# Performance work log

Hardware: AMD Instinct MI355X
Metric: run time of the kernel (lower is better)

## Reference

```python
import jax, jax.numpy as jnp
import numpy as np
from jax import lax

B, L, G, D = 32, 1024, 3, 384
H = D // 4  # hidden of attention MLPs
EPS = 1e-5


def _ln(x, g, b):
    m = x.mean(-1, keepdims=True)
    v = ((x - m) ** 2).mean(-1, keepdims=True)
    return (x - m) / jnp.sqrt(v + EPS) * g + b


def _mlp(x, W1, b1, g, beta, W2, b2):
    h = jax.nn.relu(_ln(x @ W1 + b1, g, beta))
    return h @ W2 + b2


def _forward(x, mg_W1, mg_b1, mg_g, mg_beta, mg_W2, mg_b2,
             ph_W1, ph_b1, ph_g, ph_beta, ph_W2, ph_b2,
             bd_W1, bd_b1, bd_g, bd_beta, bd_W2, bd_b2,
             cg_W1, cg_b1, cg_g, cg_beta, cg_W2, cg_b2,
             conv_W, conv_b):
    cls_tok, seq = x[:, :1, :], x[:, 1:, :]
    b = seq.shape[0]
    xg = seq.reshape(b, G, L, D)
    glob = xg.mean(axis=1, keepdims=True)                       # [b,1,L,D]
    gate_in = jnp.concatenate([xg, jnp.broadcast_to(glob, xg.shape)], axis=-1)
    gate = jax.nn.sigmoid(_mlp(gate_in, cg_W1, cg_b1, cg_g, cg_beta, cg_W2, cg_b2))  # [b,G,L,1]
    xg = xg * gate + glob * (1.0 - gate)
    # Conv2d(dim, dim, (3,1), padding=(1,0)) on [b, D, G, L]
    xc = jnp.transpose(xg, (0, 3, 1, 2))
    xc = lax.conv_general_dilated(xc, conv_W, (1, 1), ((1, 1), (0, 0)),
                                  dimension_numbers=('NCHW', 'OIHW', 'NCHW'))
    xc = xc + conv_b[None, :, None, None]
    xg = jnp.transpose(xc, (0, 2, 3, 1))                        # [b,G,L,D]
    # FFT over patch dim (vectorized over groups instead of Python loop)
    fft = jnp.fft.fft(xg, axis=2)
    mag = jnp.abs(fft)
    phase = jnp.angle(fft)
    freq = jnp.abs(jnp.fft.fftfreq(L) * L)
    r1, r2 = L // 8, L // 4
    masks = jnp.stack([(freq <= r1), (freq > r1) & (freq <= r2), (freq > r2)]).astype(mag.dtype)  # [3,L]
    bw = jax.nn.softmax(_mlp(xg.mean(axis=2), bd_W1, bd_b1, bd_g, bd_beta, bd_W2, bd_b2), axis=-1)  # [b,G,3]
    wm = jnp.einsum('bgi,il->bgl', bw, masks)[..., None]        # sum_i mask_i*band_weight_i
    mag_att = jax.nn.sigmoid(_mlp(mag, mg_W1, mg_b1, mg_g, mg_beta, mg_W2, mg_b2))
    ph_att = jnp.tanh(_mlp(phase, ph_W1, ph_b1, ph_g, ph_beta, ph_W2, ph_b2))
    mag_out = mag * wm * mag_att
    ph_out = phase * wm + ph_att
    comp = lax.complex(mag_out * jnp.cos(ph_out), mag_out * jnp.sin(ph_out))
    out = jnp.fft.ifft(comp, axis=2).real.astype(x.dtype)       # [b,G,L,D]
    out = out.reshape(b, G * L, D)
    return jnp.concatenate([cls_tok, out], axis=1)


def setup_inputs() -> dict:
    key = jax.random.key(0)
    ks = jax.random.split(key, 16)
    s = 0.02
    d = {
        'x': jax.random.normal(ks[0], (B, 1 + G * L, D), jnp.float32),
        'mg_W1': jax.random.normal(ks[1], (D, H)) * s, 'mg_b1': jnp.zeros((H,)),
        'mg_g': jnp.ones((H,)), 'mg_beta': jnp.zeros((H,)),
        'mg_W2': jax.random.normal(ks[2], (H, D)) * s, 'mg_b2': jnp.zeros((D,)),
        'ph_W1': jax.random.normal(ks[3], (D, H)) * s, 'ph_b1': jnp.zeros((H,)),
        'ph_g': jnp.ones((H,)), 'ph_beta': jnp.zeros((H,)),
        'ph_W2': jax.random.normal(ks[4], (H, D)) * s, 'ph_b2': jnp.zeros((D,)),
        'bd_W1': jax.random.normal(ks[5], (D, H)) * s, 'bd_b1': jnp.zeros((H,)),
        'bd_g': jnp.ones((H,)), 'bd_beta': jnp.zeros((H,)),
        'bd_W2': jax.random.normal(ks[6], (H, 3)) * s, 'bd_b2': jnp.zeros((3,)),
        'cg_W1': jax.random.normal(ks[7], (2 * D, D // 2)) * s, 'cg_b1': jnp.zeros((D // 2,)),
        'cg_g': jnp.ones((D // 2,)), 'cg_beta': jnp.zeros((D // 2,)),
        'cg_W2': jax.random.normal(ks[8], (D // 2, 1)) * s, 'cg_b2': jnp.zeros((1,)),
        'conv_W': jax.random.normal(ks[9], (D, D, 3, 1)) * s, 'conv_b': jnp.zeros((D,)),
    }
    return d


def reference(x, mg_W1, mg_b1, mg_g, mg_beta, mg_W2, mg_b2,
              ph_W1, ph_b1, ph_g, ph_beta, ph_W2, ph_b2,
              bd_W1, bd_b1, bd_g, bd_beta, bd_W2, bd_b2,
              cg_W1, cg_b1, cg_g, cg_beta, cg_W2, cg_b2,
              conv_W, conv_b):
    return _forward(x, mg_W1, mg_b1, mg_g, mg_beta, mg_W2, mg_b2,
                    ph_W1, ph_b1, ph_g, ph_beta, ph_W2, ph_b2,
                    bd_W1, bd_b1, bd_g, bd_beta, bd_W2, bd_b2,
                    cg_W1, cg_b1, cg_g, cg_beta, cg_W2, cg_b2,
                    conv_W, conv_b)
```

## Files before the change

### kernel.cpp

```cpp
#include <hip/hip_runtime.h>
#include <hip/hip_bf16.h>
#include <hip/hip_fp16.h>
#include <math.h>

#define NB 32
#define NL 1024
#define NG 3
#define ND 384
#define NH 96
#define NDG 192
#define SEQR 3073

typedef __attribute__((ext_vector_type(8))) short short8n;
typedef __attribute__((ext_vector_type(4))) short short4n;
typedef __attribute__((ext_vector_type(8))) _Float16 half8n;
typedef __attribute__((ext_vector_type(4))) float f32x4;
typedef __attribute__((ext_vector_type(4))) unsigned int uint4n;

__device__ __forceinline__ short bfx(float f) {
  __hip_bfloat16 h = __float2bfloat16(f);
  return *reinterpret_cast<short*>(&h);
}
__device__ __forceinline__ float xbf(short s) {
  __hip_bfloat16 h = *reinterpret_cast<__hip_bfloat16*>(&s);
  return __bfloat162float(h);
}
__device__ __forceinline__ short hfx(float f) {
  __half h = __float2half(f);
  return *reinterpret_cast<short*>(&h);
}
__device__ __forceinline__ float xhf(short s) {
  __half h = *reinterpret_cast<__half*>(&s);
  return __half2float(h);
}

__device__ __forceinline__ float fast_atan2f(float y, float x) {
  float ax = fabsf(x), ay = fabsf(y);
  float mx = fmaxf(ax, ay), mn = fminf(ax, ay);
  float r = (mx == 0.0f) ? 0.0f : __fdividef(mn, mx);
  float s = r * r;
  float p = fmaf(s, 0.0208351f, -0.0851330f);
  p = fmaf(s, p, 0.1801410f);
  p = fmaf(s, p, -0.3302995f);
  p = fmaf(s, p, 0.9998660f);
  p = r * p;
  float a = (ay > ax) ? (1.5707963267948966f - p) : p;
  a = (x < 0.0f) ? (3.14159265358979323846f - a) : a;
  return (y < 0.0f) ? -a : a;
}

__device__ __forceinline__ float fast_sigmoid(float x) {
  return __fdividef(1.0f, 1.0f + __expf(-x));
}
__device__ __forceinline__ float fast_tanh(float x) {
  return 1.0f - __fdividef(2.0f, 1.0f + __expf(2.0f * x));
}

__device__ __forceinline__ int swzd(int p) { return p + (p >> 5); }
__device__ __forceinline__ int swzt(int t) { return t + (t >> 4); }

__device__ __forceinline__ int rev4_10(int p) {
  unsigned q = (unsigned)p, r = 0;
#pragma unroll
  for (int i = 0; i < 5; i++) { r = (r << 2) | (q & 3); q >>= 2; }
  return (int)r;
}

__global__ __launch_bounds__(256) void k_prep(const float* __restrict__ convW,
                                              const float* __restrict__ x,
                                              const float* __restrict__ mgW1s,
                                              const float* __restrict__ phW1s,
                                              const float* __restrict__ mgW2s,
                                              const float* __restrict__ phW2s,
                                              const float* __restrict__ cgW1s,
                                              __hip_bfloat16* __restrict__ Wt2,
                                              float* __restrict__ twid,
                                              __half* __restrict__ W1Ao,
                                              __half* __restrict__ W2Ao,
                                              __hip_bfloat16* __restrict__ W1Go,
                                              float* __restrict__ outp) {
  int id = blockIdx.x * 256 + threadIdx.x;
  if (id < 384 * 384 * 3) {
    int i = id % 384; int rest = id / 384; int o = rest % 384; int kh = rest / 384;
    Wt2[id] = __float2bfloat16(convW[(o * 384 + i) * 3 + kh]);
    return;
  }
  int id2 = id - 384 * 384 * 3;
  if (id2 < 1024) {
    float ang = -6.283185307179586f * (float)id2 / 1024.0f;
    float s, c; sincosf(ang, &s, &c);
    twid[2 * id2] = c; twid[2 * id2 + 1] = s;
    return;
  }
  int id3 = id2 - 1024;
  if (id3 < NB * ND) {
    int b = id3 / ND, d = id3 % ND;
    outp[(size_t)b * SEQR * ND + d] = x[(size_t)b * SEQR * ND + d];
    return;
  }
  int id4 = id3 - NB * ND;
  if (id4 < 2 * 36864) {
    int br = id4 / 36864, idx = id4 % 36864;
    int j = idx & 7, ln = (idx >> 3) & 63, rest = idx >> 9;
    int f = rest % 6, kk = rest / 6;
    int m = f * 16 + (ln & 15), k = kk * 32 + (ln >> 4) * 8 + j;
    const float* W = br ? phW1s : mgW1s;
    W1Ao[id4] = __float2half(W[k * NH + m]);
    return;
  }
  int id5 = id4 - 2 * 36864;
  if (id5 < 2 * 36864) {
    int br = id5 / 36864, idx = id5 % 36864;
    int j = idx & 7, ln = (idx >> 3) & 63, rest = idx >> 9;
    int f = rest % 24, kk = rest / 24;
    int d = f * 16 + (ln & 15), k = kk * 32 + (ln >> 4) * 8 + j;
    const float* W = br ? phW2s : mgW2s;
    W2Ao[id5] = __float2half(W[k * ND + d]);
    return;
  }
  int id6 = id5 - 2 * 36864;
  if (id6 < 147456) {
    int j = id6 & 7, ln = (id6 >> 3) & 63, rest = id6 >> 9;
    int f = rest % 12, rest2 = rest / 12;
    int kk = rest2 % 12, part = rest2 / 12;
    int m = f * 16 + (ln & 15), k = part * 384 + kk * 32 + (ln >> 4) * 8 + j;
    W1Go[id6] = __float2bfloat16(cgW1s[k * NDG + m]);
  }
}

__global__ __launch_bounds__(256) void k_gate2(const float* __restrict__ x,
    const __hip_bfloat16* __restrict__ W1G,
    const float* __restrict__ b1, const float* __restrict__ gam,
    const float* __restrict__ bet, const float* __restrict__ W2,
    const float* __restrict__ b2p,
    __hip_bfloat16* __restrict__ gatedA) {
  int bid = blockIdx.x;
  int b = bid >> 6; int l0 = (bid & 63) * 16;
  int tid = threadIdx.x;
  int lane = tid & 63, wid = tid >> 6;
  int r15 = lane & 15, kc = lane >> 4;

  __shared__ short xs[3][16][392];
  __shared__ short gs[16][392];
  __shared__ float hG[16][196];
  __shared__ float s_b1[NDG], s_g[NDG], s_be[NDG], s_w2[NDG];
  __shared__ float sgate[3][16];

  if (tid < NDG) {
    s_b1[tid] = b1[tid]; s_g[tid] = gam[tid];
    s_be[tid] = bet[tid]; s_w2[tid] = W2[tid];
  }
  for (int c = tid; c < 16 * 96; c += 256) {
    int l = c / 96, d4 = (c % 96) * 4;
    size_t base = ((size_t)b * SEQR + 1 + l0 + l) * ND + d4;
    float4 v0 = *reinterpret_cast<const float4*>(&x[base]);
    float4 v1 = *reinterpret_cast<const float4*>(&x[base + (size_t)NL * ND]);
    float4 v2 = *reinterpret_cast<const float4*>(&x[base + (size_t)2 * NL * ND]);
    short4n q0, q1, q2, qg;
    q0.x = bfx(v0.x); q0.y = bfx(v0.y); q0.z = bfx(v0.z); q0.w = bfx(v0.w);
    q1.x = bfx(v1.x); q1.y = bfx(v1.y); q1.z = bfx(v1.z); q1.w = bfx(v1.w);
    q2.x = bfx(v2.x); q2.y = bfx(v2.y); q2.z = bfx(v2.z); q2.w = bfx(v2.w);
    qg.x = bfx((v0.x + v1.x + v2.x) * (1.0f / 3.0f));
    qg.y = bfx((v0.y + v1.y + v2.y) * (1.0f / 3.0f));
    qg.z = bfx((v0.z + v1.z + v2.z) * (1.0f / 3.0f));
    qg.w = bfx((v0.w + v1.w + v2.w) * (1.0f / 3.0f));
    *reinterpret_cast<short4n*>(&xs[0][l][d4]) = q0;
    *reinterpret_cast<short4n*>(&xs[1][l][d4]) = q1;
    *reinterpret_cast<short4n*>(&xs[2][l][d4]) = q2;
    *reinterpret_cast<short4n*>(&gs[l][d4]) = qg;
  }
  __syncthreads();

  const short* bsrc = (wid == 3) ? &gs[0][0] : &xs[wid][0][0];
  const __hip_bfloat16* W1b = W1G + (size_t)(wid == 3 ? 1 : 0) * 73728;
  f32x4 hacc[12];
#pragma unroll
  for (int f = 0; f < 12; f++)
#pragma unroll
    for (int j = 0; j < 4; j++)
      hacc[f][j] = (wid == 3) ? 0.0f : s_b1[f * 16 + kc * 4 + j];
  for (int kk = 0; kk < 12; kk++) {
    short8n bx = *reinterpret_cast<const short8n*>(&bsrc[r15 * 392 + kk * 32 + kc * 8]);
#pragma unroll
    for (int f = 0; f < 12; f++) {
      short8n aw = *reinterpret_cast<const short8n*>(
          (const void*)(W1b + (((size_t)kk * 12 + f) * 64 + lane) * 8));
      hacc[f] = __builtin_amdgcn_mfma_f32_16x16x32_bf16(aw, bx, hacc[f], 0, 0, 0);
    }
  }
  if (wid == 3) {
#pragma unroll
    for (int f = 0; f < 12; f++)
#pragma unroll
      for (int j = 0; j < 4; j++)
        hG[r15][f * 16 + kc * 4 + j] = hacc[f][j];
  }
  __syncthreads();
  if (wid < 3) {
    float s = 0.f, sq = 0.f;
#pragma unroll
    for (int f = 0; f < 12; f++)
#pragma unroll
      for (int j = 0; j < 4; j++) {
        float v = hacc[f][j] + hG[r15][f * 16 + kc * 4 + j];
        hacc[f][j] = v; s += v; sq += v * v;
      }
    s += __shfl_xor(s, 16, 64); s += __shfl_xor(s, 32, 64);
    sq += __shfl_xor(sq, 16, 64); sq += __shfl_xor(sq, 32, 64);
    float mean = s * (1.0f / NDG);
    float var = sq * (1.0f / NDG) - mean * mean;
    float rstd = rsqrtf(var + 1e-5f);
    float dot = 0.f;
#pragma unroll
    for (int f = 0; f < 12; f++)
#pragma unroll
      for (int j = 0; j < 4; j++) {
        int m = f * 16 + kc * 4 + j;
        float hn = fmaxf((hacc[f][j] - mean) * rstd * s_g[m] + s_be[m], 0.0f);
        dot += hn * s_w2[m];
      }
    dot += __shfl_xor(dot, 16, 64); dot += __shfl_xor(dot, 32, 64);
    float gate = fast_sigmoid(dot + b2p[0]);
    if (lane < 16) sgate[wid][r15] = gate;
  }
  __syncthreads();
  if (wid < 3) {
    size_t obase = (((size_t)b * NG + wid) * NL + l0) * ND;
    for (int c = lane; c < 16 * 96; c += 64) {
      int l = c / 96, d4 = (c % 96) * 4;
      float gt = sgate[wid][l];
      short4n qx = *reinterpret_cast<const short4n*>(&xs[wid][l][d4]);
      short4n qg = *reinterpret_cast<const short4n*>(&gs[l][d4]);
      short4n qo;
#pragma unroll
      for (int j = 0; j < 4; j++) {
        float xv = xbf(((short*)&qx)[j]);
        float gv = xbf(((short*)&qg)[j]);
        ((short*)&qo)[j] = bfx(xv * gt + gv * (1.0f - gt));
      }
      *reinterpret_cast<short4n*>(&((short*)gatedA)[obase + (size_t)l * ND + d4]) = qo;
    }
  }
}

#define BKC 64
__global__ __launch_bounds__(256) void k_conv_mfma(
    const __hip_bfloat16* __restrict__ Abuf,
    const __hip_bfloat16* __restrict__ Wt2,
    const float* __restrict__ cb,
    float* __restrict__ outp) {
  int bid = blockIdx.x;
  int ct = bid % 3; int rest = bid / 3;
  int rt = rest % 8; int bg = rest / 8;
  int b = bg / NG, gg = bg % NG;
  int l0 = rt * 128;
  int n0 = ct * 128;
  int tid = threadIdx.x;
  int lane = tid & 63, wid = tid >> 6;
  int wr = wid >> 1, wc = wid & 1;
  int r15 = lane & 15, kc = lane >> 4;

  __shared__ short As[128 * BKC];
  __shared__ short Bs[128 * BKC];

  f32x4 acc[4][4];
#pragma unroll
  for (int m = 0; m < 4; m++)
#pragma unroll
    for (int n = 0; n < 4; n++) acc[m][n] = (f32x4){0.f, 0.f, 0.f, 0.f};

  for (int kh = 0; kh < 3; kh++) {
    int gs = gg + kh - 1;
    if (gs < 0 || gs >= NG) continue;
    const __hip_bfloat16* Ag = Abuf + (((size_t)b * NG + gs) * NL + l0) * ND;
    const __hip_bfloat16* Bg = Wt2 + ((size_t)kh * 384 + n0) * 384;
    for (int k0 = 0; k0 < 384; k0 += BKC) {
      __syncthreads();
#pragma unroll
      for (int p = 0; p < 4; p++) {
        int idx = p * 256 + tid;
        int row = idx >> 3, c = idx & 7;
        int csrc = c ^ (row & 7);
        __builtin_amdgcn_global_load_lds(
            (const __attribute__((address_space(1))) void*)(Ag + (size_t)row * ND + k0 + csrc * 8),
            (__attribute__((address_space(3))) void*)(&As[idx * 8]), 16, 0, 0);
      }
#pragma unroll
      for (int p = 0; p < 4; p++) {
        int idx = p * 256 + tid;
        int row = idx >> 3, c = idx & 7;
        int csrc = c ^ (row & 7);
        __builtin_amdgcn_global_load_lds(
            (const __attribute__((address_space(1))) void*)(Bg + (size_t)row * 384 + k0 + csrc * 8),
            (__attribute__((address_space(3))) void*)(&Bs[idx * 8]), 16, 0, 0);
      }
      __syncthreads();
#pragma unroll
      for (int ks = 0; ks < 2; ks++) {
        short8n af[4], bfr[4];
        int cdata = ks * 4 + kc;
#pragma unroll
        for (int m = 0; m < 4; m++) {
          int row = wr * 64 + m * 16 + r15;
          af[m] = *reinterpret_cast<const short8n*>(&As[row * 64 + (cdata ^ (row & 7)) * 8]);
          int col = wc * 64 + m * 16 + r15;
          bfr[m] = *reinterpret_cast<const short8n*>(&Bs[col * 64 + (cdata ^ (col & 7)) * 8]);
        }
#pragma unroll
        for (int m = 0; m < 4; m++)
#pragma unroll
          for (int n = 0; n < 4; n++)
            acc[m][n] = __builtin_amdgcn_mfma_f32_16x16x32_bf16(af[m], bfr[n], acc[m][n], 0, 0, 0);
      }
    }
  }
  float cbv[4];
#pragma unroll
  for (int n = 0; n < 4; n++) cbv[n] = cb[n0 + wc * 64 + n * 16 + r15];
  size_t tbase = (size_t)(b * SEQR + 1) * ND;
#pragma unroll
  for (int n = 0; n < 4; n++) {
    int drow = gg * ND + n0 + wc * 64 + n * 16 + r15;
#pragma unroll
    for (int m = 0; m < 4; m++) {
      int lcol = l0 + wr * 64 + m * 16 + kc * 4;
      float4 v = {acc[m][n][0] + cbv[n], acc[m][n][1] + cbv[n],
                  acc[m][n][2] + cbv[n], acc[m][n][3] + cbv[n]};
      *reinterpret_cast<float4*>(&outp[tbase + (size_t)drow * NL + lcol]) = v;
    }
  }
}

__global__ __launch_bounds__(256) void k_fft_fwd(const float* __restrict__ twid,
                                                 const float* __restrict__ outp,
                                                 unsigned int* __restrict__ MG,
                                                 float* __restrict__ dcre) {
  int bid = blockIdx.x;
  int b = bid / 288;
  int rloc = (bid % 288) * 4;
  size_t rbase = (size_t)(b * SEQR + 1) * ND + (size_t)rloc * NL;
  size_t ibase = ((size_t)b * NG * ND + rloc) * NL;
  int tid = threadIdx.x;
  __shared__ float2 sc[4][1056];
  __shared__ float2 stw[816];
  for (int t = tid; t < 768; t += 256)
    stw[swzt(t)] = make_float2(twid[2 * t], twid[2 * t + 1]);
  for (int idx = tid; idx < 4096; idx += 256) {
    int line = idx >> 10, pos = idx & 1023;
    sc[line][swzd(pos)] = make_float2(outp[rbase + (size_t)line * NL + pos], 0.0f);
  }
  __syncthreads();
#pragma unroll
  for (int s2 = 8; s2 >= 0; s2 -= 2) {
    int m = 1 << s2;
    for (int bt = tid; bt < 1024; bt += 256) {
      int line = bt >> 8, j = bt & 255;
      int jj = j & (m - 1), grp = j >> s2;
      int p0 = (grp << (s2 + 2)) + jj;
      int e = jj << (8 - s2);
      float2 A = sc[line][swzd(p0)];
      float2 Bv = sc[line][swzd(p0 + m)];
      float2 Cv = sc[line][swzd(p0 + 2 * m)];
      float2 Dv = sc[line][swzd(p0 + 3 * m)];
      float t0r = A.x + Cv.x, t0i = A.y + Cv.y;
      float t1r = A.x - Cv.x, t1i = A.y - Cv.y;
      float t2r = Bv.x + Dv.x, t2i = Bv.y + Dv.y;
      float t3r = Bv.x - Dv.x, t3i = Bv.y - Dv.y;
      sc[line][swzd(p0)] = make_float2(t0r + t2r, t0i + t2i);
      float y1r = t1r + t3i, y1i = t1i - t3r;
      float y2r = t0r - t2r, y2i = t0i - t2i;
      float y3r = t1r - t3i, y3i = t1i + t3r;
      float2 w1 = stw[swzt(e)];
      float2 w2 = stw[swzt(2 * e)];
      float2 w3 = stw[swzt(3 * e)];
      sc[line][swzd(p0 + m)]     = make_float2(y1r * w1.x - y1i * w1.y, y1r * w1.y + y1i * w1.x);
      sc[line][swzd(p0 + 2 * m)] = make_float2(y2r * w2.x - y2i * w2.y, y2r * w2.y + y2i * w2.x);
      sc[line][swzd(p0 + 3 * m)] = make_float2(y3r * w3.x - y3i * w3.y, y3r * w3.y + y3i * w3.x);
    }
    __syncthreads();
  }
  for (int idx = tid; idx < 4096; idx += 256) {
    int line = idx >> 10, pos = idx & 1023;
    float2 v = sc[line][swzd(pos)];
    unsigned mg = (unsigned)(unsigned short)hfx(sqrtf(v.x * v.x + v.y * v.y));
    unsigned ph = (unsigned)(unsigned short)hfx(fast_atan2f(v.y, v.x));
    MG[ibase + (size_t)line * NL + pos] = mg | (ph << 16);
    if (pos == 0) dcre[b * NG * ND + rloc + line] = v.x;
  }
}

__global__ __launch_bounds__(256) void k_fft_inv(const float* __restrict__ twid,
                                                 unsigned int* __restrict__ MG) {
  int bid = blockIdx.x;
  int b = bid / 288;
  int rloc = (bid % 288) * 4;
  size_t ibase = ((size_t)b * NG * ND + rloc) * NL;
  int tid = threadIdx.x;
  __shared__ float2 sc[4][1056];
  __shared__ float2 stw[816];
  for (int t = tid; t < 768; t += 256)
    stw[swzt(t)] = make_float2(twid[2 * t], twid[2 * t + 1]);
  for (int idx = tid; idx < 4096; idx += 256) {
    int line = idx >> 10, pos = idx & 1023;
    unsigned w = MG[ibase + (size_t)line * NL + pos];
    float P = xhf((short)(w & 0xffff));
    float Q = xhf((short)(w >> 16));
    sc[line][swzd(pos)] = make_float2(P * __cosf(Q), P * __sinf(Q));
  }
  __syncthreads();
#pragma unroll
  for (int s2 = 0; s2 <= 8; s2 += 2) {
    int m = 1 << s2;
    for (int bt = tid; bt < 1024; bt += 256) {
      int line = bt >> 8, j = bt & 255;
      int jj = j & (m - 1), grp = j >> s2;
      int p0 = (grp << (s2 + 2)) + jj;
      int e = jj << (8 - s2);
      float2 A = sc[line][swzd(p0)];
      float2 Bv = sc[line][swzd(p0 + m)];
      float2 Cv = sc[line][swzd(p0 + 2 * m)];
      float2 Dv = sc[line][swzd(p0 + 3 * m)];
      float2 w1 = stw[swzt(e)];
      float2 w2 = stw[swzt(2 * e)];
      float2 w3 = stw[swzt(3 * e)];
      float bpr = Bv.x * w1.x + Bv.y * w1.y, bpi = Bv.y * w1.x - Bv.x * w1.y;
      float cpr = Cv.x * w2.x + Cv.y * w2.y, cpi = Cv.y * w2.x - Cv.x * w2.y;
      float dpr = Dv.x * w3.x + Dv.y * w3.y, dpi = Dv.y * w3.x - Dv.x * w3.y;
      float t0r = A.x + cpr, t0i = A.y + cpi;
      float t1r = A.x - cpr, t1i = A.y - cpi;
      float t2r = bpr + dpr, t2i = bpi + dpi;
      float er = bpr - dpr, ei = bpi - dpi;
      float t3r = -ei, t3i = er;
      sc[line][swzd(p0)]         = make_float2(t0r + t2r, t0i + t2i);
      sc[line][swzd(p0 + m)]     = make_float2(t1r + t3r, t1i + t3i);
      sc[line][swzd(p0 + 2 * m)] = make_float2(t0r - t2r, t0i - t2i);
      sc[line][swzd(p0 + 3 * m)] = make_float2(t1r - t3r, t1i - t3i);
    }
    __syncthreads();
  }
  const float scf = 1.0f / 1024.0f;
  float* realout = (float*)MG;
  for (int idx = tid; idx < 4096; idx += 256) {
    int line = idx >> 10, pos = idx & 1023;
    realout[ibase + (size_t)line * NL + pos] = sc[line][swzd(pos)].x * scf;
  }
}

__global__ __launch_bounds__(256) void k_tr(const float* __restrict__ src,
                                            float* __restrict__ dst) {
  int bid = blockIdx.x;
  int dt = bid % 6; int r1 = bid / 6;
  int lt = r1 % 16; int r2 = r1 / 16;
  int gg = r2 % NG; int b = r2 / NG;
  int tid = threadIdx.x;
  __shared__ float T[64][67];
  size_t sbase = ((size_t)b * NG * ND + gg * ND + dt * 64) * NL + lt * 64;
  for (int c = tid; c < 64 * 16; c += 256) {
    int r = c >> 4, cc = c & 15;
    float4 v = *reinterpret_cast<const float4*>(&src[sbase + (size_t)r * NL + cc * 4]);
    T[r][cc * 4 + 0] = v.x; T[r][cc * 4 + 1] = v.y;
    T[r][cc * 4 + 2] = v.z; T[r][cc * 4 + 3] = v.w;
  }
  __syncthreads();
  size_t dbase = ((size_t)b * SEQR + 1 + (size_t)gg * NL + lt * 64) * ND + dt * 64;
  for (int c = tid; c < 64 * 16; c += 256) {
    int r = c >> 4, cc = c & 15;
    float4 v = {T[cc * 4 + 0][r], T[cc * 4 + 1][r], T[cc * 4 + 2][r], T[cc * 4 + 3][r]};
    *reinterpret_cast<float4*>(&dst[dbase + (size_t)r * ND + cc * 4]) = v;
  }
}

__global__ __launch_bounds__(96) void k_bd(const float* __restrict__ dcre,
    const float* __restrict__ W1, const float* __restrict__ b1,
    const float* __restrict__ gam, const float* __restrict__ bet,
    const float* __restrict__ W2, const float* __restrict__ b2,
    float* __restrict__ bwout) {
  int bid = blockIdx.x;
  int b = bid / NG, gg = bid % NG;
  int tid = threadIdx.x;
  __shared__ float xm[ND];
  __shared__ float hs[NH];
  __shared__ float o3[3];
  const float* dc = dcre + (size_t)(b * NG + gg) * ND;
  for (int i = tid; i < ND; i += NH) xm[i] = dc[i] * (1.0f / NL);
  __syncthreads();
  float acc = b1[tid];
  for (int i = 0; i < ND; i++) acc += xm[i] * W1[i * NH + tid];
  hs[tid] = acc;
  __syncthreads();
  float s = 0, sq = 0;
  for (int i = 0; i < NH; i++) { float v = hs[i]; s += v; sq += v * v; }
  float m = s * (1.0f / NH), var = sq * (1.0f / NH) - m * m;
  float hn = fmaxf((acc - m) * rsqrtf(var + 1e-5f) * gam[tid] + bet[tid], 0.0f);
  __syncthreads();
  hs[tid] = hn;
  __syncthreads();
  if (tid < 3) {
    float o = b2[tid];
    for (int k = 0; k < NH; k++) o += hs[k] * W2[k * 3 + tid];
    o3[tid] = o;
  }
  __syncthreads();
  if (tid < 3) {
    float mx = fmaxf(o3[0], fmaxf(o3[1], o3[2]));
    float ssum = expf(o3[0] - mx) + expf(o3[1] - mx) + expf(o3[2] - mx);
    bwout[bid * 3 + tid] = expf(o3[tid] - mx) / ssum;
  }
}

#define AROW 32
#define APAD 390
__global__ __launch_bounds__(256, 3) void k_att7(
    unsigned int* __restrict__ MG,
    const __half* __restrict__ W1A,
    const __half* __restrict__ W2A,
    const float* __restrict__ mgb1, const float* __restrict__ mgg,
    const float* __restrict__ mgbe, const float* __restrict__ mgb2,
    const float* __restrict__ phb1, const float* __restrict__ phg,
    const float* __restrict__ phbe, const float* __restrict__ phb2,
    const float* __restrict__ bwp) {
  int bid = blockIdx.x;
  int bg = bid >> 5; int tile = bid & 31;
  int b = bg / NG, gg = bg % NG;
  int l0 = tile * AROW;
  int tid = threadIdx.x;
  int lane = tid & 63, wid = tid >> 6;
  int r15 = lane & 15, kc = lane >> 4;
  int br = wid >> 1;
  int wl = (wid & 1) * 16 + r15;

  __shared__ short Am[AROW * APAD];
  __shared__ short Ap[AROW * APAD];
  __shared__ short s_b1h[2][NH], s_gh[2][NH], s_beh[2][NH];
  __shared__ short s_b2h[2][ND];
  __shared__ float s_wm[AROW];

  size_t ib = ((size_t)b * NG * ND + gg * ND) * NL;

  if (tid < NH) {
    s_b1h[0][tid] = hfx(mgb1[tid]); s_b1h[1][tid] = hfx(phb1[tid]);
    s_gh[0][tid]  = hfx(mgg[tid]);  s_gh[1][tid]  = hfx(phg[tid]);
    s_beh[0][tid] = hfx(mgbe[tid]); s_beh[1][tid] = hfx(phbe[tid]);
  }
  for (int i = tid; i < ND; i += 256) { s_b2h[0][i] = hfx(mgb2[i]); s_b2h[1][i] = hfx(phb2[i]); }
  if (tid < AROW) {
    int k = rev4_10(l0 + tid);
    int fr = (k <= 512) ? k : (1024 - k);
    int bwb = (b * NG + gg) * 3;
    s_wm[tid] = (fr <= 128) ? bwp[bwb] : ((fr <= 256) ? bwp[bwb + 1] : bwp[bwb + 2]);
  }

  for (int u0 = 0; u0 < 12; u0 += 4) {
    uint4n mv[4];
#pragma unroll
    for (int u = 0; u < 4; u++) {
      int i = tid + (u0 + u) * 256;
      int d = i >> 3, lc = i & 7;
      size_t off = (size_t)d * NL + l0 + lc * 4;
      mv[u] = *reinterpret_cast<const uint4n*>(&MG[ib + off]);
    }
#pragma unroll
    for (int u = 0; u < 4; u++) {
      int i = tid + (u0 + u) * 256;
      int d = i >> 3, lc = i & 7;
#pragma unroll
      for (int j = 0; j < 4; j++) {
        int row = lc * 4 + j;
        unsigned w = mv[u][j];
        Am[row * APAD + d] = (short)(w & 0xffffu);
        Ap[row * APAD + d] = (short)(w >> 16);
      }
    }
  }
  __syncthreads();

  unsigned pk[6][2];
  {
    const short* Abuf = br ? Ap : Am;
    const __half* W1b = W1A + (size_t)br * 36864;
    f32x4 hacc[6];
#pragma unroll
    for (int f = 0; f < 6; f++) {
#pragma unroll
      for (int j = 0; j < 4; j++) hacc[f][j] = xhf(s_b1h[br][f * 16 + kc * 4 + j]);
    }
    for (int kk = 0; kk < 12; kk++) {
      half8n bx = *reinterpret_cast<const half8n*>(&Abuf[wl * APAD + kk * 32 + kc * 8]);
#pragma unroll
      for (int f = 0; f < 6; f++) {
        half8n aw = *reinterpret_cast<const half8n*>(
            (const void*)(W1b + (((size_t)kk * 6 + f) * 64 + lane) * 8));
        hacc[f] = __builtin_amdgcn_mfma_f32_16x16x32_f16(aw, bx, hacc[f], 0, 0, 0);
      }
    }
    float s = 0.f, sq = 0.f;
#pragma unroll
    for (int f = 0; f < 6; f++)
#pragma unroll
      for (int j = 0; j < 4; j++) { float v = hacc[f][j]; s += v; sq += v * v; }
    s += __shfl_xor(s, 16, 64); s += __shfl_xor(s, 32, 64);
    sq += __shfl_xor(sq, 16, 64); sq += __shfl_xor(sq, 32, 64);
    float mean = s * (1.0f / NH);
    float var = sq * (1.0f / NH) - mean * mean;
    float rstd = rsqrtf(var + 1e-5f);
#pragma unroll
    for (int f = 0; f < 6; f++) {
      float hn[4];
#pragma unroll
      for (int j = 0; j < 4; j++) {
        int m = f * 16 + kc * 4 + j;
        hn[j] = fmaxf((hacc[f][j] - mean) * rstd * xhf(s_gh[br][m]) + xhf(s_beh[br][m]), 0.0f);
      }
#pragma unroll
      for (int p = 0; p < 2; p++) {
        unsigned lo = (unsigned)(unsigned short)hfx(hn[2 * p]);
        unsigned hi = (unsigned)(unsigned short)hfx(hn[2 * p + 1]);
        pk[f][p] = lo | (hi << 16);
      }
    }
  }
  __syncthreads();

  half8n bh[3];
  {
    int srcA = r15 + ((( 2 * kc )     & 3) << 4);
    int srcB = r15 + (((2 * kc + 1) & 3) << 4);
    int hiF = kc >> 1;
#pragma unroll
    for (int kk = 0; kk < 3; kk++) {
      int a0l = __shfl((int)pk[kk * 2][0], srcA, 64);
      int a0h = __shfl((int)pk[kk * 2 + 1][0], srcA, 64);
      int a1l = __shfl((int)pk[kk * 2][1], srcA, 64);
      int a1h = __shfl((int)pk[kk * 2 + 1][1], srcA, 64);
      int b0l = __shfl((int)pk[kk * 2][0], srcB, 64);
      int b0h = __shfl((int)pk[kk * 2 + 1][0], srcB, 64);
      int b1l = __shfl((int)pk[kk * 2][1], srcB, 64);
      int b1h = __shfl((int)pk[kk * 2 + 1][1], srcB, 64);
      int4 tv;
      tv.x = hiF ? a0h : a0l;
      tv.y = hiF ? a1h : a1l;
      tv.z = hiF ? b0h : b0l;
      tv.w = hiF ? b1h : b1l;
      bh[kk] = *reinterpret_cast<half8n*>(&tv);
    }
  }

  {
    const __half* W2b = W2A + (size_t)br * 36864;
    short* stash = br ? Ap : Am;
    float wm = s_wm[wl];
#pragma unroll
    for (int chunk = 0; chunk < 4; chunk++) {
      f32x4 aX[6];
#pragma unroll
      for (int f = 0; f < 6; f++) {
        int dbase = (chunk * 6 + f) * 16 + kc * 4;
#pragma unroll
        for (int j = 0; j < 4; j++) aX[f][j] = xhf(s_b2h[br][dbase + j]);
      }
#pragma unroll
      for (int kk = 0; kk < 3; kk++) {
#pragma unroll
        for (int f = 0; f < 6; f++) {
          int fg = chunk * 6 + f;
          half8n aw = *reinterpret_cast<const half8n*>(
              (const void*)(W2b + (((size_t)kk * 24 + fg) * 64 + lane) * 8));
          aX[f] = __builtin_amdgcn_mfma_f32_16x16x32_f16(aw, bh[kk], aX[f], 0, 0, 0);
        }
      }
#pragma unroll
      for (int f = 0; f < 6; f++) {
        int dbase = (chunk * 6 + f) * 16 + kc * 4;
        short4n q;
#pragma unroll
        for (int j = 0; j < 4; j++) {
          float base = xhf(stash[wl * APAD + dbase + j]);
          float v;
          if (br) {
            v = base * wm + fast_tanh(aX[f][j]);
          } else {
            v = base * wm * fast_sigmoid(aX[f][j]);
          }
          ((short*)&q)[j] = hfx(v);
        }
        *reinterpret_cast<short4n*>(&stash[wl * APAD + dbase]) = q;
      }
    }
  }
  __syncthreads();

  for (int u = 0; u < 12; u++) {
    int i = tid + u * 256;
    int d = i >> 3, lc = i & 7;
    size_t off = (size_t)d * NL + l0 + lc * 4;
    uint4n o;
#pragma unroll
    for (int j = 0; j < 4; j++) {
      int row = lc * 4 + j;
      unsigned P = (unsigned)(unsigned short)Am[row * APAD + d];
      unsigned Q = (unsigned)(unsigned short)Ap[row * APAD + d];
      o[j] = P | (Q << 16);
    }
    *reinterpret_cast<uint4n*>(&MG[ib + off]) = o;
  }
}

extern "C" void kernel_launch(void* const* d_in, const int* in_sizes, int n_in,
                              void* d_out, int out_size, void* d_ws, size_t ws_size,
                              hipStream_t stream) {
  (void)in_sizes; (void)n_in; (void)out_size; (void)ws_size;
  const float* x     = (const float*)d_in[0];
  const float* mgW1  = (const float*)d_in[1];
  const float* mgb1  = (const float*)d_in[2];
  const float* mgg   = (const float*)d_in[3];
  const float* mgbe  = (const float*)d_in[4];
  const float* mgW2  = (const float*)d_in[5];
  const float* mgb2  = (const float*)d_in[6];
  const float* phW1  = (const float*)d_in[7];
  const float* phb1  = (const float*)d_in[8];
  const float* phg   = (const float*)d_in[9];
  const float* phbe  = (const float*)d_in[10];
  const float* phW2  = (const float*)d_in[11];
  const float* phb2  = (const float*)d_in[12];
  const float* bdW1  = (const float*)d_in[13];
  const float* bdb1  = (const float*)d_in[14];
  const float* bdg   = (const float*)d_in[15];
  const float* bdbe  = (const float*)d_in[16];
  const float* bdW2  = (const float*)d_in[17];
  const float* bdb2  = (const float*)d_in[18];
  const float* cgW1  = (const float*)d_in[19];
  const float* cgb1  = (const float*)d_in[20];
  const float* cgg   = (const float*)d_in[21];
  const float* cgbe  = (const float*)d_in[22];
  const float* cgW2  = (const float*)d_in[23];
  const float* cgb2  = (const float*)d_in[24];
  const float* convW = (const float*)d_in[25];
  const float* convB = (const float*)d_in[26];

  float* outp = (float*)d_out;
  float* wsf  = (float*)d_ws;
  unsigned int* MG = (unsigned int*)wsf;
  __hip_bfloat16* gatedA = (__hip_bfloat16*)wsf;
  char* p = (char*)(wsf + (size_t)NB * NG * NL * ND);
  __hip_bfloat16* Wt2 = (__hip_bfloat16*)p;           p += (size_t)384 * 384 * 3 * 2;
  float* twid = (float*)p;                            p += 2048 * 4;
  float* bwp  = (float*)p;                            p += 512 * 4;
  float* dcre = (float*)p;                            p += (size_t)NB * NG * ND * 4;
  __half* W1A = (__half*)p;                           p += (size_t)2 * 36864 * 2;
  __half* W2A = (__half*)p;                           p += (size_t)2 * 36864 * 2;
  __hip_bfloat16* W1G = (__hip_bfloat16*)p;           p += (size_t)147456 * 2;

  k_prep<<<dim3(2932), dim3(256), 0, stream>>>(convW, x, mgW1, phW1, mgW2, phW2, cgW1,
                                               Wt2, twid, W1A, W2A, W1G, outp);
  k_gate2<<<dim3(NB * 64), dim3(256), 0, stream>>>(x, W1G, cgb1, cgg, cgbe, cgW2, cgb2, gatedA);
  k_conv_mfma<<<dim3(NB * NG * 8 * 3), dim3(256), 0, stream>>>(gatedA, Wt2, convB, outp);
  k_fft_fwd<<<dim3(NB * 288), dim3(256), 0, stream>>>(twid, outp, MG, dcre);
  k_bd<<<dim3(NB * NG), dim3(96), 0, stream>>>(dcre, bdW1, bdb1, bdg, bdbe, bdW2, bdb2, bwp);
  k_att7<<<dim3(NB * NG * 32), dim3(256), 0, stream>>>(MG,
      W1A, W2A, mgb1, mgg, mgbe, mgb2, phb1, phg, phbe, phb2, bwp);
  k_fft_inv<<<dim3(NB * 288), dim3(256), 0, stream>>>(twid, MG);
  k_tr<<<dim3(NB * NG * 16 * 6), dim3(256), 0, stream>>>((const float*)MG, outp);
}
```

Measured before the change: 735.1 us.

## Fuse radix-4 FFT stages into register-resident radix-16 passes

Restructures the forward and inverse 1024-point FFT kernels so that each thread holds 16 complex values in registers and applies two radix-4 stages per pass (radix-16), plus a final radix-4 stage. This cuts the number of shared-memory round trips and __syncthreads barriers from five to three per FFT. It also adds a trivial-twiddle butterfly for the first inverse stage. The cost is higher register use per thread (a 4x4 float2 array) and more complex indexing, which could lower occupancy.

Result: faster. 695.3 us (-5.4%).

```diff
diff --git a/kernel.cpp b/kernel.cpp
--- a/kernel.cpp
+++ b/kernel.cpp
@@ -64,6 +64,49 @@
 #pragma unroll
   for (int i = 0; i < 5; i++) { r = (r << 2) | (q & 3); q >>= 2; }
   return (int)r;
+}
+
+__device__ __forceinline__ void bfly_dif(float2& A, float2& B, float2& C, float2& D,
+                                         float2 w1, float2 w2, float2 w3) {
+  float t0r = A.x + C.x, t0i = A.y + C.y;
+  float t1r = A.x - C.x, t1i = A.y - C.y;
+  float t2r = B.x + D.x, t2i = B.y + D.y;
+  float t3r = B.x - D.x, t3i = B.y - D.y;
+  A = make_float2(t0r + t2r, t0i + t2i);
+  float y1r = t1r + t3i, y1i = t1i - t3r;
+  float y2r = t0r - t2r, y2i = t0i - t2i;
+  float y3r = t1r - t3i, y3i = t1i + t3r;
+  B = make_float2(y1r * w1.x - y1i * w1.y, y1r * w1.y + y1i * w1.x);
+  C = make_float2(y2r * w2.x - y2i * w2.y, y2r * w2.y + y2i * w2.x);
+  D = make_float2(y3r * w3.x - y3i * w3.y, y3r * w3.y + y3i * w3.x);
+}
+
+__device__ __forceinline__ void bfly_dit(float2& A, float2& B, float2& C, float2& D,
+                                         float2 w1, float2 w2, float2 w3) {
+  float bpr = B.x * w1.x + B.y * w1.y, bpi = B.y * w1.x - B.x * w1.y;
+  float cpr = C.x * w2.x + C.y * w2.y, cpi = C.y * w2.x - C.x * w2.y;
+  float dpr = D.x * w3.x + D.y * w3.y, dpi = D.y * w3.x - D.x * w3.y;
+  float t0r = A.x + cpr, t0i = A.y + cpi;
+  float t1r = A.x - cpr, t1i = A.y - cpi;
+  float t2r = bpr + dpr, t2i = bpi + dpi;
+  float er = bpr - dpr, ei = bpi - dpi;
+  float t3r = -ei, t3i = er;
+  A = make_float2(t0r + t2r, t0i + t2i);
+  B = make_float2(t1r + t3r, t1i + t3i);
+  C = make_float2(t0r - t2r, t0i - t2i);
+  D = make_float2(t1r - t3r, t1i - t3i);
+}
+
+__device__ __forceinline__ void bfly_dit0(float2& A, float2& B, float2& C, float2& D) {
+  float t0r = A.x + C.x, t0i = A.y + C.y;
+  float t1r = A.x - C.x, t1i = A.y - C.y;
+  float t2r = B.x + D.x, t2i = B.y + D.y;
+  float er = B.x - D.x, ei = B.y - D.y;
+  float t3r = -ei, t3i = er;
+  A = make_float2(t0r + t2r, t0i + t2i);
+  B = make_float2(t1r + t3r, t1i + t3i);
+  C = make_float2(t0r - t2r, t0i - t2i);
+  D = make_float2(t1r - t3r, t1i - t3i);
 }
 
 __global__ __launch_bounds__(256) void k_prep(const float* __restrict__ convW,
@@ -350,42 +393,87 @@
     sc[line][swzd(pos)] = make_float2(outp[rbase + (size_t)line * NL + pos], 0.0f);
   }
   __syncthreads();
-#pragma unroll
-  for (int s2 = 8; s2 >= 0; s2 -= 2) {
-    int m = 1 << s2;
-    for (int bt = tid; bt < 1024; bt += 256) {
-      int line = bt >> 8, j = bt & 255;
-      int jj = j & (m - 1), grp = j >> s2;
-      int p0 = (grp << (s2 + 2)) + jj;
-      int e = jj << (8 - s2);
-      float2 A = sc[line][swzd(p0)];
-      float2 Bv = sc[line][swzd(p0 + m)];
-      float2 Cv = sc[line][swzd(p0 + 2 * m)];
-      float2 Dv = sc[line][swzd(p0 + 3 * m)];
-      float t0r = A.x + Cv.x, t0i = A.y + Cv.y;
-      float t1r = A.x - Cv.x, t1i = A.y - Cv.y;
-      float t2r = Bv.x + Dv.x, t2i = Bv.y + Dv.y;
-      float t3r = Bv.x - Dv.x, t3i = Bv.y - Dv.y;
-      sc[line][swzd(p0)] = make_float2(t0r + t2r, t0i + t2i);
-      float y1r = t1r + t3i, y1i = t1i - t3r;
-      float y2r = t0r - t2r, y2i = t0i - t2i;
-      float y3r = t1r - t3i, y3i = t1i + t3r;
-      float2 w1 = stw[swzt(e)];
-      float2 w2 = stw[swzt(2 * e)];
-      float2 w3 = stw[swzt(3 * e)];
-      sc[line][swzd(p0 + m)]     = make_float2(y1r * w1.x - y1i * w1.y, y1r * w1.y + y1i * w1.x);
-      sc[line][swzd(p0 + 2 * m)] = make_float2(y2r * w2.x - y2i * w2.y, y2r * w2.y + y2i * w2.x);
-      sc[line][swzd(p0 + 3 * m)] = make_float2(y3r * w3.x - y3i * w3.y, y3r * w3.y + y3i * w3.x);
-    }
-    __syncthreads();
-  }
+  int line = tid >> 6;
+  {
+    int jjp = tid & 63;
+    float2 X[4][4];
+#pragma unroll
+    for (int a = 0; a < 4; a++)
+#pragma unroll
+      for (int c = 0; c < 4; c++)
+        X[a][c] = sc[line][swzd(a * 256 + c * 64 + jjp)];
+#pragma unroll
+    for (int c = 0; c < 4; c++) {
+      int e = c * 64 + jjp;
+      bfly_dif(X[0][c], X[1][c], X[2][c], X[3][c],
+               stw[swzt(e)], stw[swzt(2 * e)], stw[swzt(3 * e)]);
+    }
+    {
+      int e = jjp << 2;
+      float2 w1 = stw[swzt(e)], w2 = stw[swzt(2 * e)], w3 = stw[swzt(3 * e)];
+#pragma unroll
+      for (int a = 0; a < 4; a++)
+        bfly_dif(X[a][0], X[a][1], X[a][2], X[a][3], w1, w2, w3);
+    }
+#pragma unroll
+    for (int a = 0; a < 4; a++)
+#pragma unroll
+      for (int c = 0; c < 4; c++)
+        sc[line][swzd(a * 256 + c * 64 + jjp)] = X[a][c];
+  }
+  __syncthreads();
+  {
+    int idx = tid & 63;
+    int g = idx >> 2, jjp = idx & 3;
+    int base = g * 64 + jjp;
+    float2 X[4][4];
+#pragma unroll
+    for (int a = 0; a < 4; a++)
+#pragma unroll
+      for (int c = 0; c < 4; c++)
+        X[a][c] = sc[line][swzd(base + a * 16 + c * 4)];
+#pragma unroll
+    for (int c = 0; c < 4; c++) {
+      int e = (c * 4 + jjp) << 4;
+      bfly_dif(X[0][c], X[1][c], X[2][c], X[3][c],
+               stw[swzt(e)], stw[swzt(2 * e)], stw[swzt(3 * e)]);
+    }
+    {
+      int e = jjp << 6;
+      float2 w1 = stw[swzt(e)], w2 = stw[swzt(2 * e)], w3 = stw[swzt(3 * e)];
+#pragma unroll
+      for (int a = 0; a < 4; a++)
+        bfly_dif(X[a][0], X[a][1], X[a][2], X[a][3], w1, w2, w3);
+    }
+#pragma unroll
+    for (int a = 0; a < 4; a++)
+#pragma unroll
+      for (int c = 0; c < 4; c++)
+        sc[line][swzd(base + a * 16 + c * 4)] = X[a][c];
+  }
+  __syncthreads();
+#pragma unroll
+  for (int u = 0; u < 4; u++) {
+    int p0 = tid * 4;
+    float2 A = sc[u][swzd(p0)], B = sc[u][swzd(p0 + 1)];
+    float2 C = sc[u][swzd(p0 + 2)], D = sc[u][swzd(p0 + 3)];
+    float t0r = A.x + C.x, t0i = A.y + C.y;
+    float t1r = A.x - C.x, t1i = A.y - C.y;
+    float t2r = B.x + D.x, t2i = B.y + D.y;
+    float t3r = B.x - D.x, t3i = B.y - D.y;
+    sc[u][swzd(p0)]     = make_float2(t0r + t2r, t0i + t2i);
+    sc[u][swzd(p0 + 1)] = make_float2(t1r + t3i, t1i - t3r);
+    sc[u][swzd(p0 + 2)] = make_float2(t0r - t2r, t0i - t2i);
+    sc[u][swzd(p0 + 3)] = make_float2(t1r - t3i, t1i + t3r);
+  }
+  __syncthreads();
   for (int idx = tid; idx < 4096; idx += 256) {
-    int line = idx >> 10, pos = idx & 1023;
-    float2 v = sc[line][swzd(pos)];
+    int li = idx >> 10, pos = idx & 1023;
+    float2 v = sc[li][swzd(pos)];
     unsigned mg = (unsigned)(unsigned short)hfx(sqrtf(v.x * v.x + v.y * v.y));
     unsigned ph = (unsigned)(unsigned short)hfx(fast_atan2f(v.y, v.x));
-    MG[ibase + (size_t)line * NL + pos] = mg | (ph << 16);
-    if (pos == 0) dcre[b * NG * ND + rloc + line] = v.x;
+    MG[ibase + (size_t)li * NL + pos] = mg | (ph << 16);
+    if (pos == 0) dcre[b * NG * ND + rloc + li] = v.x;
   }
 }
 
@@ -408,41 +496,78 @@
     sc[line][swzd(pos)] = make_float2(P * __cosf(Q), P * __sinf(Q));
   }
   __syncthreads();
-#pragma unroll
-  for (int s2 = 0; s2 <= 8; s2 += 2) {
-    int m = 1 << s2;
-    for (int bt = tid; bt < 1024; bt += 256) {
-      int line = bt >> 8, j = bt & 255;
-      int jj = j & (m - 1), grp = j >> s2;
-      int p0 = (grp << (s2 + 2)) + jj;
-      int e = jj << (8 - s2);
-      float2 A = sc[line][swzd(p0)];
-      float2 Bv = sc[line][swzd(p0 + m)];
-      float2 Cv = sc[line][swzd(p0 + 2 * m)];
-      float2 Dv = sc[line][swzd(p0 + 3 * m)];
-      float2 w1 = stw[swzt(e)];
-      float2 w2 = stw[swzt(2 * e)];
-      float2 w3 = stw[swzt(3 * e)];
-      float bpr = Bv.x * w1.x + Bv.y * w1.y, bpi = Bv.y * w1.x - Bv.x * w1.y;
-      float cpr = Cv.x * w2.x + Cv.y * w2.y, cpi = Cv.y * w2.x - Cv.x * w2.y;
-      float dpr = Dv.x * w3.x + Dv.y * w3.y, dpi = Dv.y * w3.x - Dv.x * w3.y;
-      float t0r = A.x + cpr, t0i = A.y + cpi;
-      float t1r = A.x - cpr, t1i = A.y - cpi;
-      float t2r = bpr + dpr, t2i = bpi + dpi;
-      float er = bpr - dpr, ei = bpi - dpi;
-      float t3r = -ei, t3i = er;
-      sc[line][swzd(p0)]         = make_float2(t0r + t2r, t0i + t2i);
-      sc[line][swzd(p0 + m)]     = make_float2(t1r + t3r, t1i + t3i);
-      sc[line][swzd(p0 + 2 * m)] = make_float2(t0r - t2r, t0i - t2i);
-      sc[line][swzd(p0 + 3 * m)] = make_float2(t1r - t3r, t1i - t3i);
-    }
-    __syncthreads();
-  }
+  int line = tid >> 6;
+  {
+    int G = tid & 63;
+    int base = G * 16;
+    float2 X[4][4];
+#pragma unroll
+    for (int q = 0; q < 4; q++)
+#pragma unroll
+      for (int r = 0; r < 4; r++)
+        X[q][r] = sc[line][swzd(base + q * 4 + r)];
+#pragma unroll
+    for (int q = 0; q < 4; q++)
+      bfly_dit0(X[q][0], X[q][1], X[q][2], X[q][3]);
+#pragma unroll
+    for (int r = 0; r < 4; r++) {
+      int e = r << 6;
+      bfly_dit(X[0][r], X[1][r], X[2][r], X[3][r],
+               stw[swzt(e)], stw[swzt(2 * e)], stw[swzt(3 * e)]);
+    }
+#pragma unroll
+    for (int q = 0; q < 4; q++)
+#pragma unroll
+      for (int r = 0; r < 4; r++)
+        sc[line][swzd(base + q * 4 + r)] = X[q][r];
+  }
+  __syncthreads();
+  {
+    int idx = tid & 63;
+    int G = idx >> 4, jj = idx & 15;
+    int base = G * 256 + jj;
+    float2 X[4][4];
+#pragma unroll
+    for (int k = 0; k < 4; k++)
+#pragma unroll
+      for (int u = 0; u < 4; u++)
+        X[k][u] = sc[line][swzd(base + u * 64 + k * 16)];
+    {
+      int e = jj << 4;
+      float2 w1 = stw[swzt(e)], w2 = stw[swzt(2 * e)], w3 = stw[swzt(3 * e)];
+#pragma unroll
+      for (int u = 0; u < 4; u++)
+        bfly_dit(X[0][u], X[1][u], X[2][u], X[3][u], w1, w2, w3);
+    }
+#pragma unroll
+    for (int k = 0; k < 4; k++) {
+      int e = (k * 16 + jj) << 2;
+      bfly_dit(X[k][0], X[k][1], X[k][2], X[k][3],
+               stw[swzt(e)], stw[swzt(2 * e)], stw[swzt(3 * e)]);
+    }
+#pragma unroll
+    for (int k = 0; k < 4; k++)
+#pragma unroll
+      for (int u = 0; u < 4; u++)
+        sc[line][swzd(base + u * 64 + k * 16)] = X[k][u];
+  }
+  __syncthreads();
+#pragma unroll
+  for (int u = 0; u < 4; u++) {
+    int jj = tid;
+    int e = jj;
+    float2 A = sc[u][swzd(jj)],       B = sc[u][swzd(jj + 256)];
+    float2 C = sc[u][swzd(jj + 512)], D = sc[u][swzd(jj + 768)];
+    bfly_dit(A, B, C, D, stw[swzt(e)], stw[swzt(2 * e)], stw[swzt(3 * e)]);
+    sc[u][swzd(jj)] = A; sc[u][swzd(jj + 256)] = B;
+    sc[u][swzd(jj + 512)] = C; sc[u][swzd(jj + 768)] = D;
+  }
+  __syncthreads();
   const float scf = 1.0f / 1024.0f;
   float* realout = (float*)MG;
   for (int idx = tid; idx < 4096; idx += 256) {
-    int line = idx >> 10, pos = idx & 1023;
-    realout[ibase + (size_t)line * NL + pos] = sc[line][swzd(pos)].x * scf;
+    int li = idx >> 10, pos = idx & 1023;
+    realout[ibase + (size_t)li * NL + pos] = sc[li][swzd(pos)].x * scf;
   }
 }
 
```
